# Performance work log

Hardware: AMD Instinct MI355X
Metric: run time of the kernel (lower is better)

Reference implementation:

```python
import jax, jax.numpy as jnp
import numpy as np

H = 1024   # lstm hidden size
F = 512    # feature dim
P = 66     # pose dim
T_IN = 10
T_OUT = 25


def _glorot(key, shape):
    fan = shape[-1]
    return jax.random.normal(key, shape, dtype=jnp.float32) / np.sqrt(fan)


def setup_inputs() -> dict:
    key = jax.random.key(0)
    ks = jax.random.split(key, 24)
    B = 256
    inp = {
        'x': jax.random.normal(ks[0], (B, T_IN, P), dtype=jnp.float32),
        'z': jax.random.normal(ks[1], (B, T_IN, P), dtype=jnp.float32),
        'for_resid': jax.random.normal(ks[2], (B, T_OUT, P), dtype=jnp.float32),
        # ToFeature: Linear(66 -> 512)
        'tf_w': _glorot(ks[3], (F, P)), 'tf_b': jnp.zeros((F,), jnp.float32),
        # encoder LSTM(512 -> 1024)
        'enc_wih': _glorot(ks[4], (4 * H, F)), 'enc_whh': _glorot(ks[5], (4 * H, H)),
        'enc_bih': jnp.zeros((4 * H,), jnp.float32), 'enc_bhh': jnp.zeros((4 * H,), jnp.float32),
        # encoder_post LSTM(512 -> 1024)
        'encp_wih': _glorot(ks[6], (4 * H, F)), 'encp_whh': _glorot(ks[7], (4 * H, H)),
        'encp_bih': jnp.zeros((4 * H,), jnp.float32), 'encp_bhh': jnp.zeros((4 * H,), jnp.float32),
        # decoder cell LSTM(512 -> 1024)
        'dec_wih': _glorot(ks[8], (4 * H, F)), 'dec_whh': _glorot(ks[9], (4 * H, H)),
        'dec_bih': jnp.zeros((4 * H,), jnp.float32), 'dec_bhh': jnp.zeros((4 * H,), jnp.float32),
        # decoder lin: Linear(1024 -> 512)
        'lin_w': _glorot(ks[10], (F, H)), 'lin_b': jnp.zeros((F,), jnp.float32),
        # ToPose: Linear(1024 -> 66)
        'tp_w': _glorot(ks[11], (P, H)), 'tp_b': jnp.zeros((P,), jnp.float32),
    }
    return inp


def _lstm_step(h, c, xt, wih, whh, bih, bhh):
    gates = xt @ wih.T + bih + h @ whh.T + bhh  # (B, 4H)
    i, f, g, o = jnp.split(gates, 4, axis=-1)
    c_new = jax.nn.sigmoid(f) * c + jax.nn.sigmoid(i) * jnp.tanh(g)
    h_new = jax.nn.sigmoid(o) * jnp.tanh(c_new)
    return h_new, c_new


def _lstm_scan(xs, wih, whh, bih, bhh):
    # xs: (T, B, I)
    B = xs.shape[1]
    h0 = jnp.zeros((B, H), xs.dtype)
    c0 = jnp.zeros((B, H), xs.dtype)

    def step(carry, xt):
        h, c = carry
        h, c = _lstm_step(h, c, xt, wih, whh, bih, bhh)
        return (h, c), h

    (h_n, c_n), all_h = jax.lax.scan(step, (h0, c0), xs)
    return all_h, h_n, c_n


def reference(x, z, for_resid, tf_w, tf_b,
              enc_wih, enc_whh, enc_bih, enc_bhh,
              encp_wih, encp_whh, encp_bih, encp_bhh,
              dec_wih, dec_whh, dec_bih, dec_bhh,
              lin_w, lin_b, tp_w, tp_b):
    # ToFeature + permute to time-major (T, B, F)
    xf = jnp.transpose(x @ tf_w.T + tf_b, (1, 0, 2))
    zf = jnp.transpose(z @ tf_w.T + tf_b, (1, 0, 2))

    all_h, h_n, c_n = _lstm_scan(xf, enc_wih, enc_whh, enc_bih, enc_bhh)   # (10,B,H)
    all_hz, _, _ = _lstm_scan(zf, encp_wih, encp_whh, encp_bih, encp_bhh)  # (10,B,H)

    def dec_step(carry, _):
        h, c = carry                                   # (B,H), (B,H)
        cat_h = jnp.concatenate([all_h, h[None], all_hz], axis=0)  # (21,B,H)
        scores = jnp.einsum('bh,tbh->tb', c, cat_h)
        attw = jax.nn.softmax(scores, axis=0)
        atth = jnp.einsum('tb,tbh->bh', attw, cat_h)   # attention context -> LSTM h0
        inp = h @ lin_w.T + lin_b                      # (B,F)
        h_new, c_new = _lstm_step(atth, c, inp, dec_wih, dec_whh, dec_bih, dec_bhh)
        return (h_new, c_new), h_new

    _, dec_hs = jax.lax.scan(dec_step, (h_n, c_n), None, length=T_OUT)  # (25,B,H)
    out = jnp.transpose(dec_hs, (1, 0, 2))             # (B,25,H)
    o = out @ tp_w.T + tp_b                            # (B,25,66)
    return o + for_resid
```

## Files before the change

### kernel.cpp

```cpp
#include <hip/hip_runtime.h>
#include <hip/hip_bf16.h>
#include <hip/hip_cooperative_groups.h>

namespace cg = cooperative_groups;

#define DEV __device__ __forceinline__

typedef unsigned short u16;
typedef short bf16x8_t __attribute__((ext_vector_type(8)));
typedef float f32x4_t __attribute__((ext_vector_type(4)));

constexpr int NBLK = 256;
constexpr int NTHR = 512;
constexpr int NT_ALL = NBLK * NTHR;
constexpr size_t HSTRIDE = 256 * 1024;
constexpr int SMEM_BYTES = 98304;

struct Params {
  const float *x, *z, *resid, *tf_w, *tf_b;
  const float *e_wih, *e_whh, *e_bih, *e_bhh;
  const float *p_wih, *p_whh, *p_bih, *p_bhh;
  const float *d_wih, *d_whh, *d_bih, *d_bhh;
  const float *lin_w, *lin_b, *tp_w, *tp_b;
  u16 *Wenc, *Wencp, *Wdec, *wihP, *linT, *tpw;
  float *bias_e, *bias_ep, *bias_d, *bias_part;
  u16 *xf, *zf;
  u16 *he, *hp;
  u16 *hs;
  u16 *atth;
  float *c_pub;
  unsigned *bar;
  float *out;
};

DEV float b2f(u16 v) { unsigned u = ((unsigned)v) << 16; float f; __builtin_memcpy(&f, &u, 4); return f; }
DEV u16 f2b(float f) {
  unsigned u; __builtin_memcpy(&u, &f, 4);
  unsigned r = u + 0x7fffu + ((u >> 16) & 1u);
  return (u16)(r >> 16);
}
DEV unsigned pk2(float a, float b) { return (unsigned)f2b(a) | ((unsigned)f2b(b) << 16); }
DEV uint4 cvt8(const float* s) {
  float4 a = *(const float4*)s;
  float4 b = *(const float4*)(s + 4);
  uint4 r;
  r.x = pk2(a.x, a.y); r.y = pk2(a.z, a.w);
  r.z = pk2(b.x, b.y); r.w = pk2(b.z, b.w);
  return r;
}
DEV float sigm(float x) { return 1.0f / (1.0f + __expf(-x)); }
DEV f32x4_t fzero4() { f32x4_t v = {0.f, 0.f, 0.f, 0.f}; return v; }

DEV void gll16(const void* g, void* l) {
  __builtin_amdgcn_global_load_lds(
      (const __attribute__((address_space(1))) void*)g,
      (__attribute__((address_space(3))) void*)l, 16, 0, 0);
}

template <typename T> DEV void st_wt(T* p, T v) {
  __hip_atomic_store(p, v, __ATOMIC_RELAXED, __HIP_MEMORY_SCOPE_AGENT);
}
template <typename T> DEV T ld_byp(const T* p) {
  return __hip_atomic_load(p, __ATOMIC_RELAXED, __HIP_MEMORY_SCOPE_AGENT);
}

DEV void fullbar(unsigned* ctrs, int bid, unsigned tgt, int tid) {
  asm volatile("s_waitcnt vmcnt(0)" ::: "memory");
  __syncthreads();
  if (tid == 0) atomicAdd(&ctrs[(bid & 7) * 16], 1u);
  if (tid < 8) { while (ld_byp(&ctrs[tid * 16]) < tgt) __builtin_amdgcn_s_sleep(2); }
  __syncthreads();
}
DEV void gbar(unsigned* ctrs, int cbase, int myidx, unsigned tgt, int tid) {
  asm volatile("s_waitcnt vmcnt(0)" ::: "memory");
  __syncthreads();
  if (tid == 0) atomicAdd(&ctrs[(cbase + myidx) * 16], 1u);
  if (tid < 4) { while (ld_byp(&ctrs[(cbase + tid) * 16]) < tgt) __builtin_amdgcn_s_sleep(2); }
  __syncthreads();
}
DEV void lanebar8(unsigned* ctrs, int lane, int j, unsigned tgt, int tid) {
  asm volatile("s_waitcnt vmcnt(0)" ::: "memory");
  __syncthreads();
  if (tid == 0) atomicAdd(&ctrs[(16 + lane * 8 + (j & 7)) * 16], 1u);
  if (tid < 8) { while (ld_byp(&ctrs[(16 + lane * 8 + tid) * 16]) < tgt) __builtin_amdgcn_s_sleep(1); }
  __syncthreads();
}

template <int PM>
DEV void gemm128(const u16* __restrict__ xa, int ldx, int xcols,
                 const u16* __restrict__ ha, int ldh,
                 const u16* __restrict__ wsrc, int ldw, int K,
                 int m0, int n0, int tid, char* sm, f32x4_t acc[4]) {
  char* lA = sm;
  char* lB = sm + 32768;
  const int NK = K >> 6;
  const int row = tid >> 3;
  const int usw = ((tid & 7) ^ (row & 7)) * 8;
  const int wv = tid >> 6;
  char* laD = lA + (wv << 10);
  char* lbD = lB + (wv << 10);
  const u16* aX = xa + (size_t)(m0 + row) * ldx + usw;
  const u16* aH = ha + (size_t)(m0 + row) * ldh + usw - xcols;
  const u16* bW0 = wsrc + (size_t)(n0 + row) * ldw + usw;
  const u16* bW1 = bW0 + (size_t)64 * ldw;

  auto sA = [&](int ks) {
    const int k0 = ks << 6;
    const u16* g = (k0 < xcols) ? (aX + k0) : (aH + k0);
    gll16(g, laD + (((ks + 2) & 3) << 13));
  };
  auto sB = [&](int ks) {
    const int k0 = ks << 6;
    const int so = ((ks + 2) & 3) << 14;
    gll16(bW0 + k0, lbD + so);
    gll16(bW1 + k0, lbD + so + 8192);
  };

  const int l = tid & 63, l15 = l & 15, lhi = l >> 4;
  const int wr = wv >> 2, wc = wv & 3;
  const int rA0 = wr * 32 + l15, rA1 = rA0 + 16;
  const int nB0 = wc * 32 + l15, nB1 = nB0 + 16;
  const int a00 = rA0 * 128 + ((lhi ^ (rA0 & 7)) << 4);
  const int a01 = rA0 * 128 + (((lhi + 4) ^ (rA0 & 7)) << 4);
  const int a10 = rA1 * 128 + ((lhi ^ (rA1 & 7)) << 4);
  const int a11 = rA1 * 128 + (((lhi + 4) ^ (rA1 & 7)) << 4);
  const int b00 = nB0 * 128 + ((lhi ^ (nB0 & 7)) << 4);
  const int b01 = nB0 * 128 + (((lhi + 4) ^ (nB0 & 7)) << 4);
  const int b10 = nB1 * 128 + ((lhi ^ (nB1 & 7)) << 4);
  const int b11 = nB1 * 128 + (((lhi + 4) ^ (nB1 & 7)) << 4);

  if (PM == 0) { sA(0); sB(0); sA(1); sB(1); }

#pragma unroll 1
  for (int ks = 0; ks < NK; ++ks) {
    if (ks + 2 < NK) { sA(ks + 2); sB(ks + 2); }
    if (ks + 2 < NK)        asm volatile("s_waitcnt vmcnt(6)" ::: "memory");
    else if (ks + 2 == NK)  asm volatile("s_waitcnt vmcnt(3)" ::: "memory");
    else                    asm volatile("s_waitcnt vmcnt(0)" ::: "memory");
    __builtin_amdgcn_s_barrier();
    const char* A  = lA + (((ks + 2) & 3) << 13);
    const char* Bq = lB + (((ks + 2) & 3) << 14);
#pragma unroll
    for (int kh = 0; kh < 2; ++kh) {
      bf16x8_t va0 = *(const bf16x8_t*)(A + (kh ? a01 : a00));
      bf16x8_t va1 = *(const bf16x8_t*)(A + (kh ? a11 : a10));
      bf16x8_t vb0 = *(const bf16x8_t*)(Bq + (kh ? b01 : b00));
      bf16x8_t vb1 = *(const bf16x8_t*)(Bq + (kh ? b11 : b10));
      acc[0] = __builtin_amdgcn_mfma_f32_16x16x32_bf16(va0, vb0, acc[0], 0, 0, 0);
      acc[1] = __builtin_amdgcn_mfma_f32_16x16x32_bf16(va0, vb1, acc[1], 0, 0, 0);
      acc[2] = __builtin_amdgcn_mfma_f32_16x16x32_bf16(va1, vb0, acc[2], 0, 0, 0);
      acc[3] = __builtin_amdgcn_mfma_f32_16x16x32_bf16(va1, vb1, acc[3], 0, 0, 0);
    }
  }
  asm volatile("s_waitcnt lgkmcnt(0)" ::: "memory");
  __builtin_amdgcn_s_barrier();
}

DEV void preA128(const u16* src, int lds_, int m0, int tid, char* sm, int ks) {
  const int row = tid >> 3, usw = ((tid & 7) ^ (row & 7)) * 8, wv = tid >> 6;
  gll16(src + (size_t)(m0 + row) * lds_ + (ks << 6) + usw,
        sm + (wv << 10) + (((ks + 2) & 3) << 13));
}
DEV void preB128(const u16* w, int ldw, int n0, int tid, char* sm, int ks) {
  const int row = tid >> 3, usw = ((tid & 7) ^ (row & 7)) * 8, wv = tid >> 6;
  char* d = sm + 32768 + (wv << 10) + (((ks + 2) & 3) << 14);
  gll16(w + (size_t)(n0 + row) * ldw + (ks << 6) + usw, d);
  gll16(w + (size_t)(n0 + 64 + row) * ldw + (ks << 6) + usw, d + 8192);
}

DEV void gemm64d(const u16* __restrict__ a, int lda,
                 const u16* __restrict__ w, int ldw, int K,
                 int m0, int n0, int tid, char* sm, f32x4_t acc[2]) {
  char* lB = sm;
  char* lA = sm + 32768;
  const int NK = K >> 6;
  const int row = tid >> 3, uu = tid & 7;
  const int usw = uu ^ (row & 7);
  const int wv = tid >> 6;
  char* la_base = lA + (wv << 10);
  char* lb_base = lB + (wv << 10);
  const u16* aS = a + (size_t)(m0 + row) * lda + usw * 8;
  const u16* bS = w + (size_t)(n0 + row) * ldw + usw * 8;

  auto stageA = [&](int ks) { gll16(aS + (ks << 6), la_base + ((ks & 3) << 13)); };
  auto stage  = [&](int ks) {
    gll16(aS + (ks << 6), la_base + ((ks & 3) << 13));
    gll16(bS + (ks << 6), lb_base + ((ks & 3) << 13));
  };

  const int l = tid & 63, l15 = l & 15, lhi = l >> 4;
  const int wr = wv >> 1, wc = wv & 1;
  const int rA = wr * 16 + l15;
  const int aoff0 = rA * 128 + ((lhi ^ (rA & 7)) << 4);
  const int aoff1 = rA * 128 + (((lhi + 4) ^ (rA & 7)) << 4);
  const int nB0 = wc * 32 + l15, nB1 = nB0 + 16;
  const int boff00 = nB0 * 128 + ((lhi ^ (nB0 & 7)) << 4);
  const int boff01 = nB0 * 128 + (((lhi + 4) ^ (nB0 & 7)) << 4);
  const int boff10 = nB1 * 128 + ((lhi ^ (nB1 & 7)) << 4);
  const int boff11 = nB1 * 128 + (((lhi + 4) ^ (nB1 & 7)) << 4);

  stageA(0); stageA(1);

#pragma unroll 1
  for (int ks = 0; ks < NK; ++ks) {
    if (ks + 2 < NK) stage(ks + 2);
    if (ks == 0)            asm volatile("s_waitcnt vmcnt(3)" ::: "memory");
    else if (ks + 2 < NK)   asm volatile("s_waitcnt vmcnt(4)" ::: "memory");
    else if (ks + 2 == NK)  asm volatile("s_waitcnt vmcnt(2)" ::: "memory");
    else                    asm volatile("s_waitcnt vmcnt(0)" ::: "memory");
    __builtin_amdgcn_s_barrier();
    const char* A  = lA + ((ks & 3) << 13);
    const char* Bb = lB + ((ks & 3) << 13);
    bf16x8_t a0  = *(const bf16x8_t*)(A + aoff0);
    bf16x8_t a1  = *(const bf16x8_t*)(A + aoff1);
    bf16x8_t b00 = *(const bf16x8_t*)(Bb + boff00);
    bf16x8_t b01 = *(const bf16x8_t*)(Bb + boff01);
    bf16x8_t b10 = *(const bf16x8_t*)(Bb + boff10);
    bf16x8_t b11 = *(const bf16x8_t*)(Bb + boff11);
    acc[0] = __builtin_amdgcn_mfma_f32_16x16x32_bf16(a0, b00, acc[0], 0, 0, 0);
    acc[0] = __builtin_amdgcn_mfma_f32_16x16x32_bf16(a1, b01, acc[0], 0, 0, 0);
    acc[1] = __builtin_amdgcn_mfma_f32_16x16x32_bf16(a0, b10, acc[1], 0, 0, 0);
    acc[1] = __builtin_amdgcn_mfma_f32_16x16x32_bf16(a1, b11, acc[1], 0, 0, 0);
  }
  asm volatile("s_waitcnt lgkmcnt(0)" ::: "memory");
  __builtin_amdgcn_s_barrier();
}

DEV void preB64(const u16* w, int ldw, int n0, int tid, char* sm, int ks) {
  const int row = tid >> 3, usw = (tid & 7) ^ (row & 7), wv = tid >> 6;
  gll16(w + (size_t)(n0 + row) * ldw + (ks << 6) + usw * 8,
        sm + (wv << 10) + ((ks & 3) << 13));
}

DEV void lstm_ep128(const f32x4_t acc[4], int tid, char* sm,
                    const float* __restrict__ bias, float cc[4],
                    u16* __restrict__ hw, float* __restrict__ cpub,
                    int m0, int n0) {
  float* gl = (float*)sm;
  const int l = tid & 63, l15 = l & 15, lhi = l >> 4;
  const int wv = tid >> 6, wr = wv >> 2, wc = wv & 3;
#pragma unroll
  for (int mf = 0; mf < 2; ++mf)
#pragma unroll
    for (int nf = 0; nf < 2; ++nf)
#pragma unroll
      for (int qq = 0; qq < 4; ++qq)
        gl[(wr * 32 + mf * 16 + lhi * 4 + qq) * 128 + wc * 32 + nf * 16 + l15] =
            acc[mf * 2 + nf][qq];
  __syncthreads();
#pragma unroll
  for (int it = 0; it < 4; ++it) {
    int idx = it * 512 + tid;
    int r = idx >> 5, jj = idx & 31;
    f32x4_t g4 = *(const f32x4_t*)(gl + r * 128 + jj * 4);
    f32x4_t b4 = *(const f32x4_t*)(bias + n0 + jj * 4);
    float ig = sigm(g4[0] + b4[0]);
    float fg = sigm(g4[1] + b4[1]);
    float g_ = tanhf(g4[2] + b4[2]);
    float og = sigm(g4[3] + b4[3]);
    float cn = fg * cc[it] + ig * g_;
    cc[it] = cn;
    float hn = og * tanhf(cn);
    size_t off = (size_t)(m0 + r) * 1024 + (n0 >> 2) + jj;
    st_wt(&hw[off], f2b(hn));
    if (cpub) st_wt(&cpub[off], cn);
  }
  __syncthreads();
}

DEV void lstm_ep64(const f32x4_t acc[2], int tid, char* sm,
                   const float* __restrict__ bias, float cc[2],
                   const float* __restrict__ cinit,
                   u16* __restrict__ hw, float* __restrict__ cpub,
                   int m0, int n0) {
  float* gl = (float*)(sm + 49152);
  const int l = tid & 63, l15 = l & 15, lhi = l >> 4;
  const int wv = tid >> 6, wr = wv >> 1, wc = wv & 1;
#pragma unroll
  for (int jf = 0; jf < 2; ++jf)
#pragma unroll
    for (int qq = 0; qq < 4; ++qq)
      gl[(wr * 16 + lhi * 4 + qq) * 64 + wc * 32 + jf * 16 + l15] = acc[jf][qq];
  __syncthreads();
#pragma unroll
  for (int it = 0; it < 2; ++it) {
    int idx = it * 512 + tid;
    int r = idx >> 4, jj = idx & 15;
    f32x4_t g4 = *(const f32x4_t*)(gl + r * 64 + jj * 4);
    f32x4_t b4 = *(const f32x4_t*)(bias + n0 + jj * 4);
    float ig = sigm(g4[0] + b4[0]);
    float fg = sigm(g4[1] + b4[1]);
    float g_ = tanhf(g4[2] + b4[2]);
    float og = sigm(g4[3] + b4[3]);
    size_t off = (size_t)(m0 + r) * 1024 + (n0 >> 2) + jj;
    float cold = cinit ? ld_byp(cinit + off) : cc[it];
    float cn = fg * cold + ig * g_;
    cc[it] = cn;
    float hn = og * tanhf(cn);
    st_wt(&hw[off], f2b(hn));
    if (cpub) st_wt(&cpub[off], cn);
  }
  __syncthreads();
}

DEV void wx_store(const f32x4_t acc[4], int tid, u16* __restrict__ Wdec,
                  int m0, int n0) {
  const int l = tid & 63, l15 = l & 15, lhi = l >> 4;
  const int wv = tid >> 6, wr = wv >> 2, wc = wv & 3;
#pragma unroll
  for (int mf = 0; mf < 2; ++mf)
#pragma unroll
    for (int nf = 0; nf < 2; ++nf)
#pragma unroll
      for (int qq = 0; qq < 4; ++qq) {
        int r = m0 + wr * 32 + mf * 16 + lhi * 4 + qq;
        int c = n0 + wc * 32 + nf * 16 + l15;
        st_wt(&Wdec[(size_t)r * 2048 + c], f2b(acc[mf * 2 + nf][qq]));
      }
}

DEV void phase0_tf(const Params& p, int bid, int tid, char* sm) {
  float* xs = (float*)sm;
  float* zs = (float*)(sm + 2688);
  for (int g = tid; g < 660; g += NTHR) {
    int t = g / 66, qd = g - t * 66;
    xs[g] = p.x[((size_t)bid * 10 + t) * 66 + qd];
    zs[g] = p.z[((size_t)bid * 10 + t) * 66 + qd];
  }
  __syncthreads();
  const int n = tid;
  float accx[10], accz[10];
  float bn = p.tf_b[n];
#pragma unroll
  for (int t = 0; t < 10; ++t) { accx[t] = bn; accz[t] = bn; }
  const float* wrow = p.tf_w + (size_t)n * 66;
  for (int k = 0; k < 66; ++k) {
    float wk = wrow[k];
#pragma unroll
    for (int t = 0; t < 10; ++t) {
      accx[t] = fmaf(wk, xs[t * 66 + k], accx[t]);
      accz[t] = fmaf(wk, zs[t * 66 + k], accz[t]);
    }
  }
#pragma unroll
  for (int t = 0; t < 10; ++t) {
    p.xf[(size_t)t * 131072 + (size_t)bid * 512 + n] = f2b(accx[t]);
    p.zf[(size_t)t * 131072 + (size_t)bid * 512 + n] = f2b(accz[t]);
  }
  __syncthreads();
}

DEV void phase0a(const Params& p, int gtid) {
  for (int g = gtid; g < 786432; g += NT_ALL) {
    int row = g / 192;
    int u = g - row * 192;
    int k = u * 8;
    int nsrc = (row & 3) * 1024 + (row >> 2);
    const float* s1 = (k < 512) ? (p.e_wih + (size_t)nsrc * 512 + k)
                                : (p.e_whh + (size_t)nsrc * 1024 + (k - 512));
    ((uint4*)p.Wenc)[g] = cvt8(s1);
    const float* s2 = (k < 512) ? (p.p_wih + (size_t)nsrc * 512 + k)
                                : (p.p_whh + (size_t)nsrc * 1024 + (k - 512));
    ((uint4*)p.Wencp)[g] = cvt8(s2);
  }
  for (int g = gtid; g < 524288; g += NT_ALL) {
    int row = g >> 7, u = g & 127;
    int nsrc = (row & 3) * 1024 + (row >> 2);
    ((uint4*)p.Wdec)[row * 256 + 128 + u] = cvt8(p.d_whh + (size_t)nsrc * 1024 + u * 8);
  }
  for (int g = gtid; g < 262144; g += NT_ALL) {
    int row = g >> 6, u = g & 63;
    int nsrc = (row & 3) * 1024 + (row >> 2);
    ((uint4*)p.wihP)[g] = cvt8(p.d_wih + (size_t)nsrc * 512 + u * 8);
  }
  for (int g = gtid; g < 524288; g += NT_ALL) {
    int f = g >> 10, h = g & 1023;
    p.linT[(size_t)h * 512 + f] = f2b(p.lin_w[g]);
  }
  for (int g = gtid; g < 8448; g += NT_ALL)
    ((uint4*)p.tpw)[g] = cvt8(p.tp_w + g * 8);
  for (int g = gtid; g < 4096; g += NT_ALL) {
    int nsrc = (g & 3) * 1024 + (g >> 2);
    p.bias_e[g]  = p.e_bih[nsrc] + p.e_bhh[nsrc];
    p.bias_ep[g] = p.p_bih[nsrc] + p.p_bhh[nsrc];
  }
  for (int g = gtid; g < 32768; g += NT_ALL) {
    int cell = g >> 3, sub = g & 7;
    int nsrc = (cell & 3) * 1024 + (cell >> 2);
    const float* wr_ = p.d_wih + (size_t)nsrc * 512 + sub * 64;
    const float* lb = p.lin_b + sub * 64;
    float s = 0.f;
    for (int f = 0; f < 64; ++f) s += wr_[f] * lb[f];
    p.bias_part[g] = s;
  }
  uint4 zz; zz.x = zz.y = zz.z = zz.w = 0u;
  for (int g = gtid; g < 32768; g += NT_ALL) { ((uint4*)p.he)[g] = zz; ((uint4*)p.hp)[g] = zz; }
}

DEV void attention(const Params& p, const u16* hd_prev, const float* cpub,
                   u16* atth_s, int b, int tid, char* sm) {
  u16*   catl = (u16*)(sm + 16384);
  float* cl   = (float*)(sm + 59392);
  float* sc   = (float*)(sm + 63488);
  for (int g = tid; g < 2688; g += NTHR) {
    int t = g >> 7, hu = g & 127;
    const u16* src;
    if (t < 10)       src = p.he + (size_t)(t + 1) * HSTRIDE;
    else if (t == 10) src = hd_prev;
    else              src = p.hp + (size_t)(t - 10) * HSTRIDE;
    ((uint4*)catl)[g] = *(const uint4*)(src + (size_t)b * 1024 + hu * 8);
  }
  for (int g = tid; g < 512; g += NTHR) {
    unsigned long long v = ld_byp(((const unsigned long long*)(cpub + (size_t)b * 1024)) + g);
    ((unsigned long long*)cl)[g] = v;
  }
  __syncthreads();
  const int wv = tid >> 6, l = tid & 63;
  for (int t = wv; t < 21; t += 8) {
    float s = 0.f;
    const u16* cr = catl + t * 1024;
    for (int hh = l; hh < 1024; hh += 64) s += cl[hh] * b2f(cr[hh]);
#pragma unroll
    for (int o = 32; o; o >>= 1) s += __shfl_down(s, o);
    if (l == 0) sc[t] = s;
  }
  __syncthreads();
  float m = -1e30f;
#pragma unroll
  for (int t = 0; t < 21; ++t) m = fmaxf(m, sc[t]);
  float e[21]; float den = 0.f;
#pragma unroll
  for (int t = 0; t < 21; ++t) { e[t] = __expf(sc[t] - m); den += e[t]; }
  float inv = 1.0f / den;
  const int h0 = tid * 2;
  float a0 = 0.f, a1 = 0.f;
#pragma unroll
  for (int t = 0; t < 21; ++t) {
    float w_ = e[t] * inv;
    unsigned v = *(const unsigned*)(catl + t * 1024 + h0);
    a0 += w_ * b2f((u16)(v & 0xffff));
    a1 += w_ * b2f((u16)(v >> 16));
  }
  st_wt(((unsigned*)(atth_s + (size_t)b * 1024)) + tid, pk2(a0, a1));
  __syncthreads();
}

DEV void finalproj(const Params& p, int b, int tid, char* sm) {
  u16* hl = (u16*)sm;
  for (int g = tid; g < 3200; g += NTHR) {
    int t = g >> 7, hu = g & 127;
    ((uint4*)hl)[g] = *(const uint4*)(p.hs + ((size_t)(t * 256 + b)) * 1024 + hu * 8);
  }
  __syncthreads();
  if (tid < 330) {
    int pcol = tid % 66, tg = tid / 66;
    float acc[5] = {0.f, 0.f, 0.f, 0.f, 0.f};
    const u16* wrow = p.tpw + (size_t)pcol * 1024;
    for (int hc = 0; hc < 128; ++hc) {
      uint4 wv4 = ((const uint4*)wrow)[hc];
      float wf[8];
      wf[0] = b2f(wv4.x & 0xffff); wf[1] = b2f(wv4.x >> 16);
      wf[2] = b2f(wv4.y & 0xffff); wf[3] = b2f(wv4.y >> 16);
      wf[4] = b2f(wv4.z & 0xffff); wf[5] = b2f(wv4.z >> 16);
      wf[6] = b2f(wv4.w & 0xffff); wf[7] = b2f(wv4.w >> 16);
#pragma unroll
      for (int r = 0; r < 5; ++r) {
        int t = tg * 5 + r;
        uint4 hv = ((const uint4*)(hl + t * 1024))[hc];
        float s;
        s  = wf[0] * b2f(hv.x & 0xffff) + wf[1] * b2f(hv.x >> 16);
        s += wf[2] * b2f(hv.y & 0xffff) + wf[3] * b2f(hv.y >> 16);
        s += wf[4] * b2f(hv.z & 0xffff) + wf[5] * b2f(hv.z >> 16);
        s += wf[6] * b2f(hv.w & 0xffff) + wf[7] * b2f(hv.w >> 16);
        acc[r] += s;
      }
    }
    float bb = p.tp_b[pcol];
#pragma unroll
    for (int r = 0; r < 5; ++r) {
      int t = tg * 5 + r;
      size_t o = (size_t)b * 1650 + (size_t)t * 66 + pcol;
      p.out[o] = acc[r] + bb + p.resid[o];
    }
  }
}

__global__ __launch_bounds__(NTHR) void model_kernel(Params p) {
  cg::grid_group gg = cg::this_grid();
  extern __shared__ __align__(16) char sm[];
  const int tid = threadIdx.x;
  const int bid = blockIdx.x;
  const int gtid = bid * NTHR + tid;

  phase0_tf(p, bid, tid, sm);
  phase0a(p, gtid);
  if (bid == 0 && tid < 48) st_wt(&p.bar[tid * 16], 0u);
  gg.sync();

  for (int g = gtid; g < 4096; g += NT_ALL) {
    int nsrc = (g & 3) * 1024 + (g >> 2);
    float s = p.d_bih[nsrc] + p.d_bhh[nsrc];
#pragma unroll
    for (int k8 = 0; k8 < 8; ++k8) s += p.bias_part[g * 8 + k8];
    st_wt(&p.bias_d[g], s);
  }

#pragma unroll 1
  for (int i = 0; i < 2; ++i) {
    int tt = bid * 2 + i;
    int m0w = (tt & 63) << 6;
    int n0w = (tt >> 6) << 7;
    f32x4_t acc[4] = {fzero4(), fzero4(), fzero4(), fzero4()};
    gemm128<0>(p.wihP, 512, 512, p.wihP, 512, p.linT, 512, 512,
               m0w, n0w, tid, sm, acc);
    wx_store(acc, tid, p.Wdec, m0w, n0w);
  }

  const int grp = bid >> 7;
  const int q = bid & 127;
  const int m0e = (q >> 5) << 6;
  const int n0e = (q & 31) << 7;
  const int cb = grp ? 12 : 8;
  const int cidx = q >> 5;

  const int lane = bid >> 6, j = bid & 63;
  const int m0d = lane << 6;
  const int n0d = ((j & 7) * 8 + (j >> 3)) << 6;

  const u16* xsrc = grp ? p.zf : p.xf;
  const u16* Wg   = grp ? p.Wencp : p.Wenc;
  u16* hbuf       = grp ? p.hp : p.he;
  const float* bias_g = grp ? p.bias_ep : p.bias_e;

  preA128(xsrc, 512, m0e, tid, sm, 0);
  preB128(Wg, 1536, n0e, tid, sm, 0);
  preA128(xsrc, 512, m0e, tid, sm, 1);
  preB128(Wg, 1536, n0e, tid, sm, 1);
  fullbar(p.bar, bid, 32u, tid);

  float cc[4] = {0.f, 0.f, 0.f, 0.f};

#pragma unroll 1
  for (int t = 0; t < 10; ++t) {
    f32x4_t acc[4] = {fzero4(), fzero4(), fzero4(), fzero4()};
    gemm128<1>(xsrc + (size_t)t * 131072, 512, 512, hbuf + (size_t)t * HSTRIDE, 1024,
               Wg, 1536, 1536, m0e, n0e, tid, sm, acc);
    lstm_ep128(acc, tid, sm, bias_g, cc, hbuf + (size_t)(t + 1) * HSTRIDE,
               (!grp && t == 9) ? p.c_pub : (float*)0, m0e, n0e);
    if (t < 9) {
      preA128(xsrc + (size_t)(t + 1) * 131072, 512, m0e, tid, sm, 0);
      preB128(Wg, 1536, n0e, tid, sm, 0);
      preA128(xsrc + (size_t)(t + 1) * 131072, 512, m0e, tid, sm, 1);
      preB128(Wg, 1536, n0e, tid, sm, 1);
    } else {
      preB64(p.Wdec, 2048, n0d, tid, sm, 0);
      preB64(p.Wdec, 2048, n0d, tid, sm, 1);
    }
    gbar(p.bar, cb, cidx, (unsigned)(t + 1) * 32, tid);
  }
  fullbar(p.bar, bid, 64u, tid);

  float cd[2] = {0.f, 0.f};
  unsigned lep = 0;
#pragma unroll 1
  for (int s = 0; s < 25; ++s) {
    const u16* hd_prev = (s == 0) ? (p.he + (size_t)10 * HSTRIDE)
                                  : (p.hs + (size_t)(s - 1) * HSTRIDE);
    u16* atth_s = p.atth + (size_t)s * HSTRIDE;
    attention(p, hd_prev, p.c_pub + (size_t)(s & 1) * 262144, atth_s, bid, tid, sm);
    f32x4_t acc[2]; acc[0] = fzero4(); acc[1] = fzero4();
    gemm64d(hd_prev, 1024, p.Wdec, 2048, 1024, m0d, n0d, tid, sm, acc);
    preB64(p.Wdec + 1024, 2048, n0d, tid, sm, 0);
    preB64(p.Wdec + 1024, 2048, n0d, tid, sm, 1);
    ++lep; lanebar8(p.bar, lane, j, lep * 8u, tid);
    gemm64d(atth_s, 1024, p.Wdec + 1024, 2048, 1024, m0d, n0d, tid, sm, acc);
    lstm_ep64(acc, tid, sm, p.bias_d, cd,
              (s == 0) ? p.c_pub : (const float*)0,
              p.hs + (size_t)s * HSTRIDE,
              p.c_pub + (size_t)((s + 1) & 1) * 262144, m0d, n0d);
    if (s < 24) {
      preB64(p.Wdec, 2048, n0d, tid, sm, 0);
      preB64(p.Wdec, 2048, n0d, tid, sm, 1);
    }
    ++lep; lanebar8(p.bar, lane, j, lep * 8u, tid);
  }

  finalproj(p, bid, tid, sm);
}

extern "C" void kernel_launch(void* const* d_in, const int* in_sizes, int n_in,
                              void* d_out, int out_size, void* d_ws, size_t ws_size,
                              hipStream_t stream) {
  (void)in_sizes; (void)n_in; (void)out_size;
  Params P;
  P.x     = (const float*)d_in[0];
  P.z     = (const float*)d_in[1];
  P.resid = (const float*)d_in[2];
  P.tf_w  = (const float*)d_in[3];
  P.tf_b  = (const float*)d_in[4];
  P.e_wih = (const float*)d_in[5];
  P.e_whh = (const float*)d_in[6];
  P.e_bih = (const float*)d_in[7];
  P.e_bhh = (const float*)d_in[8];
  P.p_wih = (const float*)d_in[9];
  P.p_whh = (const float*)d_in[10];
  P.p_bih = (const float*)d_in[11];
  P.p_bhh = (const float*)d_in[12];
  P.d_wih = (const float*)d_in[13];
  P.d_whh = (const float*)d_in[14];
  P.d_bih = (const float*)d_in[15];
  P.d_bhh = (const float*)d_in[16];
  P.lin_w = (const float*)d_in[17];
  P.lin_b = (const float*)d_in[18];
  P.tp_w  = (const float*)d_in[19];
  P.tp_b  = (const float*)d_in[20];

  char* w = (char*)d_ws;
  size_t o = 0;
  auto take = [&](size_t bytes) { char* r = w + o; o = (o + bytes + 255) & ~(size_t)255; return r; };
  P.Wenc  = (u16*)take(4096ull * 1536 * 2);
  P.Wencp = (u16*)take(4096ull * 1536 * 2);
  P.Wdec  = (u16*)take(4096ull * 2048 * 2);
  P.wihP  = (u16*)take(4096ull * 512 * 2);
  P.linT  = (u16*)take(1024ull * 512 * 2);
  P.tpw   = (u16*)take(66ull * 1024 * 2);
  P.bias_e    = (float*)take(4096 * 4);
  P.bias_ep   = (float*)take(4096 * 4);
  P.bias_d    = (float*)take(4096 * 4);
  P.bias_part = (float*)take(32768 * 4);
  P.xf  = (u16*)take(10ull * 256 * 512 * 2);
  P.zf  = (u16*)take(10ull * 256 * 512 * 2);
  P.he  = (u16*)take(11ull * 256 * 1024 * 2);
  P.hp  = (u16*)take(11ull * 256 * 1024 * 2);
  P.hs  = (u16*)take(25ull * 256 * 1024 * 2);
  P.atth = (u16*)take(25ull * 256 * 1024 * 2);
  P.c_pub = (float*)take(2ull * 256 * 1024 * 4);
  P.bar   = (unsigned*)take(48 * 64);
  P.out = (float*)d_out;

  if (o > ws_size) return;

  hipFuncSetAttribute((const void*)model_kernel,
                      hipFuncAttributeMaxDynamicSharedMemorySize, SMEM_BYTES);

  void* args[] = { &P };
  hipLaunchCooperativeKernel((const void*)model_kernel, dim3(NBLK, 1, 1),
                             dim3(NTHR, 1, 1), args, SMEM_BYTES, stream);
}
```

Before: 840.5 us.

## Replace atomic-counter barriers with per-block epoch slots and cache attention history in LDS

Grid and lane barriers now use per-block epoch slots. Each block writes its own slot with a plain store, and waiters poll all slots, instead of doing atomicAdd on shared counters. The encoder hidden-state history for attention is loaded into a larger LDS region once after the encoder, so each decoder step only refreshes the newest decoder h row rather than reloading all 21 rows. The decoder GEMM's A-operand prefetch is issued before attention so the loads overlap it. In exchange, LDS use rises, which may affect occupancy, and each barrier now polls many more slots.

```diff
diff --git a/kernel.cpp b/kernel.cpp
--- a/kernel.cpp
+++ b/kernel.cpp
@@ -14,7 +14,10 @@
 constexpr int NTHR = 512;
 constexpr int NT_ALL = NBLK * NTHR;
 constexpr size_t HSTRIDE = 256 * 1024;
-constexpr int SMEM_BYTES = 98304;
+constexpr int SMEM_BYTES = 147456;
+constexpr int CATL_OFF = 98304;
+constexpr int CL_OFF   = 141312;
+constexpr int SC_OFF   = 145408;
 
 struct Params {
   const float *x, *z, *resid, *tf_w, *tf_b;
@@ -64,25 +67,12 @@
   return __hip_atomic_load(p, __ATOMIC_RELAXED, __HIP_MEMORY_SCOPE_AGENT);
 }
 
-DEV void fullbar(unsigned* ctrs, int bid, unsigned tgt, int tid) {
+DEV void sbar(unsigned* slots, int base, int idx, int n, unsigned ep, int tid) {
   asm volatile("s_waitcnt vmcnt(0)" ::: "memory");
   __syncthreads();
-  if (tid == 0) atomicAdd(&ctrs[(bid & 7) * 16], 1u);
-  if (tid < 8) { while (ld_byp(&ctrs[tid * 16]) < tgt) __builtin_amdgcn_s_sleep(2); }
-  __syncthreads();
-}
-DEV void gbar(unsigned* ctrs, int cbase, int myidx, unsigned tgt, int tid) {
-  asm volatile("s_waitcnt vmcnt(0)" ::: "memory");
-  __syncthreads();
-  if (tid == 0) atomicAdd(&ctrs[(cbase + myidx) * 16], 1u);
-  if (tid < 4) { while (ld_byp(&ctrs[(cbase + tid) * 16]) < tgt) __builtin_amdgcn_s_sleep(2); }
-  __syncthreads();
-}
-DEV void lanebar8(unsigned* ctrs, int lane, int j, unsigned tgt, int tid) {
-  asm volatile("s_waitcnt vmcnt(0)" ::: "memory");
-  __syncthreads();
-  if (tid == 0) atomicAdd(&ctrs[(16 + lane * 8 + (j & 7)) * 16], 1u);
-  if (tid < 8) { while (ld_byp(&ctrs[(16 + lane * 8 + tid) * 16]) < tgt) __builtin_amdgcn_s_sleep(1); }
+  if (tid == 0) st_wt(&slots[(base + idx) * 16], ep);
+  for (int i = tid; i < n; i += NTHR)
+    while (ld_byp(&slots[(base + i) * 16]) < ep) __builtin_amdgcn_s_sleep(2);
   __syncthreads();
 }
 
@@ -168,6 +158,7 @@
   gll16(w + (size_t)(n0 + 64 + row) * ldw + (ks << 6) + usw, d + 8192);
 }
 
+template <int PRE>
 DEV void gemm64d(const u16* __restrict__ a, int lda,
                  const u16* __restrict__ w, int ldw, int K,
                  int m0, int n0, int tid, char* sm, f32x4_t acc[2]) {
@@ -199,12 +190,15 @@
   const int boff10 = nB1 * 128 + ((lhi ^ (nB1 & 7)) << 4);
   const int boff11 = nB1 * 128 + (((lhi + 4) ^ (nB1 & 7)) << 4);
 
-  stageA(0); stageA(1);
+  if (PRE == 0) { stageA(0); stageA(1); }
 
 #pragma unroll 1
   for (int ks = 0; ks < NK; ++ks) {
     if (ks + 2 < NK) stage(ks + 2);
-    if (ks == 0)            asm volatile("s_waitcnt vmcnt(3)" ::: "memory");
+    if (ks == 0) {
+      if (PRE == 0) asm volatile("s_waitcnt vmcnt(3)" ::: "memory");
+      else          asm volatile("s_waitcnt vmcnt(2)" ::: "memory");
+    }
     else if (ks + 2 < NK)   asm volatile("s_waitcnt vmcnt(4)" ::: "memory");
     else if (ks + 2 == NK)  asm volatile("s_waitcnt vmcnt(2)" ::: "memory");
     else                    asm volatile("s_waitcnt vmcnt(0)" ::: "memory");
@@ -231,6 +225,11 @@
   gll16(w + (size_t)(n0 + row) * ldw + (ks << 6) + usw * 8,
         sm + (wv << 10) + ((ks & 3) << 13));
 }
+DEV void preA64(const u16* a, int lda, int m0, int tid, char* sm, int ks) {
+  const int row = tid >> 3, usw = (tid & 7) ^ (row & 7), wv = tid >> 6;
+  gll16(a + (size_t)(m0 + row) * lda + (ks << 6) + usw * 8,
+        sm + 32768 + (wv << 10) + ((ks & 3) << 13));
+}
 
 DEV void lstm_ep128(const f32x4_t acc[4], int tid, char* sm,
                     const float* __restrict__ bias, float cc[4],
@@ -273,7 +272,7 @@
                    const float* __restrict__ cinit,
                    u16* __restrict__ hw, float* __restrict__ cpub,
                    int m0, int n0) {
-  float* gl = (float*)(sm + 49152);
+  float* gl = (float*)(sm + 65536);
   const int l = tid & 63, l15 = l & 15, lhi = l >> 4;
   const int wv = tid >> 6, wr = wv >> 1, wc = wv & 1;
 #pragma unroll
@@ -397,18 +396,14 @@
   for (int g = gtid; g < 32768; g += NT_ALL) { ((uint4*)p.he)[g] = zz; ((uint4*)p.hp)[g] = zz; }
 }
 
-DEV void attention(const Params& p, const u16* hd_prev, const float* cpub,
-                   u16* atth_s, int b, int tid, char* sm) {
-  u16*   catl = (u16*)(sm + 16384);
-  float* cl   = (float*)(sm + 59392);
-  float* sc   = (float*)(sm + 63488);
-  for (int g = tid; g < 2688; g += NTHR) {
-    int t = g >> 7, hu = g & 127;
-    const u16* src;
-    if (t < 10)       src = p.he + (size_t)(t + 1) * HSTRIDE;
-    else if (t == 10) src = hd_prev;
-    else              src = p.hp + (size_t)(t - 10) * HSTRIDE;
-    ((uint4*)catl)[g] = *(const uint4*)(src + (size_t)b * 1024 + hu * 8);
+DEV void attention2(const u16* hd_prev, const float* cpub, u16* atth_s,
+                    int b, int tid, char* sm, bool refresh) {
+  u16*   catl = (u16*)(sm + CATL_OFF);
+  float* cl   = (float*)(sm + CL_OFF);
+  float* sc   = (float*)(sm + SC_OFF);
+  if (refresh) {
+    for (int g = tid; g < 128; g += NTHR)
+      ((uint4*)catl)[10 * 128 + g] = *(const uint4*)(hd_prev + (size_t)b * 1024 + g * 8);
   }
   for (int g = tid; g < 512; g += NTHR) {
     unsigned long long v = ld_byp(((const unsigned long long*)(cpub + (size_t)b * 1024)) + g);
@@ -442,7 +437,6 @@
     a1 += w_ * b2f((u16)(v >> 16));
   }
   st_wt(((unsigned*)(atth_s + (size_t)b * 1024)) + tid, pk2(a0, a1));
-  __syncthreads();
 }
 
 DEV void finalproj(const Params& p, int b, int tid, char* sm) {
@@ -494,7 +488,8 @@
 
   phase0_tf(p, bid, tid, sm);
   phase0a(p, gtid);
-  if (bid == 0 && tid < 48) st_wt(&p.bar[tid * 16], 0u);
+  if (bid == 0)
+    for (int g = tid; g < 768; g += NTHR) st_wt(&p.bar[g * 16], 0u);
   gg.sync();
 
   for (int g = gtid; g < 4096; g += NT_ALL) {
@@ -520,8 +515,6 @@
   const int q = bid & 127;
   const int m0e = (q >> 5) << 6;
   const int n0e = (q & 31) << 7;
-  const int cb = grp ? 12 : 8;
-  const int cidx = q >> 5;
 
   const int lane = bid >> 6, j = bid & 63;
   const int m0d = lane << 6;
@@ -536,7 +529,7 @@
   preB128(Wg, 1536, n0e, tid, sm, 0);
   preA128(xsrc, 512, m0e, tid, sm, 1);
   preB128(Wg, 1536, n0e, tid, sm, 1);
-  fullbar(p.bar, bid, 32u, tid);
+  sbar(p.bar, 0, bid, 256, 1u, tid);
 
   float cc[4] = {0.f, 0.f, 0.f, 0.f};
 
@@ -556,9 +549,21 @@
       preB64(p.Wdec, 2048, n0d, tid, sm, 0);
       preB64(p.Wdec, 2048, n0d, tid, sm, 1);
     }
-    gbar(p.bar, cb, cidx, (unsigned)(t + 1) * 32, tid);
-  }
-  fullbar(p.bar, bid, 64u, tid);
+    sbar(p.bar, 256 + grp * 128, q, 128, (unsigned)(t + 1), tid);
+  }
+  sbar(p.bar, 0, bid, 256, 2u, tid);
+
+  {
+    u16* catl = (u16*)(sm + CATL_OFF);
+    for (int g = tid; g < 2688; g += NTHR) {
+      int t = g >> 7, hu = g & 127;
+      const u16* src;
+      if (t < 10)       src = p.he + (size_t)(t + 1) * HSTRIDE;
+      else if (t == 10) src = p.he + (size_t)10 * HSTRIDE;
+      else              src = p.hp + (size_t)(t - 10) * HSTRIDE;
+      ((uint4*)catl)[g] = *(const uint4*)(src + (size_t)bid * 1024 + hu * 8);
+    }
+  }
 
   float cd[2] = {0.f, 0.f};
   unsigned lep = 0;
@@ -567,13 +572,15 @@
     const u16* hd_prev = (s == 0) ? (p.he + (size_t)10 * HSTRIDE)
                                   : (p.hs + (size_t)(s - 1) * HSTRIDE);
     u16* atth_s = p.atth + (size_t)s * HSTRIDE;
-    attention(p, hd_prev, p.c_pub + (size_t)(s & 1) * 262144, atth_s, bid, tid, sm);
+    preA64(hd_prev, 1024, m0d, tid, sm, 0);
+    preA64(hd_prev, 1024, m0d, tid, sm, 1);
+    attention2(hd_prev, p.c_pub + (size_t)(s & 1) * 262144, atth_s, bid, tid, sm, s > 0);
     f32x4_t acc[2]; acc[0] = fzero4(); acc[1] = fzero4();
-    gemm64d(hd_prev, 1024, p.Wdec, 2048, 1024, m0d, n0d, tid, sm, acc);
+    gemm64d<1>(hd_prev, 1024, p.Wdec, 2048, 1024, m0d, n0d, tid, sm, acc);
     preB64(p.Wdec + 1024, 2048, n0d, tid, sm, 0);
     preB64(p.Wdec + 1024, 2048, n0d, tid, sm, 1);
-    ++lep; lanebar8(p.bar, lane, j, lep * 8u, tid);
-    gemm64d(atth_s, 1024, p.Wdec + 1024, 2048, 1024, m0d, n0d, tid, sm, acc);
+    ++lep; sbar(p.bar, 512 + lane * 64, j, 64, lep, tid);
+    gemm64d<0>(atth_s, 1024, p.Wdec + 1024, 2048, 1024, m0d, n0d, tid, sm, acc);
     lstm_ep64(acc, tid, sm, p.bias_d, cd,
               (s == 0) ? p.c_pub : (const float*)0,
               p.hs + (size_t)s * HSTRIDE,
@@ -582,7 +589,7 @@
       preB64(p.Wdec, 2048, n0d, tid, sm, 0);
       preB64(p.Wdec, 2048, n0d, tid, sm, 1);
     }
-    ++lep; lanebar8(p.bar, lane, j, lep * 8u, tid);
+    ++lep; sbar(p.bar, 512 + lane * 64, j, 64, lep, tid);
   }
 
   finalproj(p, bid, tid, sm);
@@ -635,7 +642,7 @@
   P.hs  = (u16*)take(25ull * 256 * 1024 * 2);
   P.atth = (u16*)take(25ull * 256 * 1024 * 2);
   P.c_pub = (float*)take(2ull * 256 * 1024 * 4);
-  P.bar   = (unsigned*)take(48 * 64);
+  P.bar   = (unsigned*)take(768 * 64);
   P.out = (float*)d_out;
 
   if (o > ws_size) return;
```

Result: faster. 735.6 us (-12.5%).
